# Performance work log

Hardware: AMD Instinct MI355X
Metric: run time of the kernel (lower is better)

## Reference

```python
import jax, jax.numpy as jnp
import numpy as np

N = 50000      # nodes
E = 800000     # edges (before self-loops)
DIN = 2        # dim_input
DEMB = 128     # dim_embedding
H = 8          # n_heads
DV = 16        # dim_values (H*DV == DEMB)
DH = 512       # dim_hidden
L = 2          # n_att_layers
K = 10         # APPNP steps
ALPHA = 0.1
EPS = 1e-5     # BatchNorm eps
NEG_SLOPE = 0.2  # GAT leaky_relu slope


def setup_inputs() -> dict:
    key = jax.random.key(0)
    ks = jax.random.split(key, 16)
    s = 0.05
    inp = {}
    inp["x"] = jax.random.normal(ks[0], (N, DIN), jnp.float32)
    inp["J"] = jax.random.uniform(ks[1], (N, 1), jnp.float32)
    inp["edge_index"] = jax.random.randint(ks[2], (2, E), 0, N, jnp.int32)
    # Lin1: Linear(dim_input+1, dim_embedding)
    inp["lin0_w"] = jax.random.normal(ks[3], (DIN + 1, DEMB), jnp.float32) * s
    inp["lin0_b"] = jnp.zeros((DEMB,), jnp.float32)
    # Per attention layer (stacked over L):
    inp["gat_w"]   = jax.random.normal(ks[4], (L, DEMB, H * DV), jnp.float32) * s
    inp["att_src"] = jax.random.normal(ks[5], (L, H, DV), jnp.float32) * s
    inp["att_dst"] = jax.random.normal(ks[6], (L, H, DV), jnp.float32) * s
    inp["lin1_w"]  = jax.random.normal(ks[7], (L, DV, DEMB), jnp.float32) * s
    inp["bn1_g"]   = jnp.ones((L, DEMB), jnp.float32)
    inp["bn1_b"]   = jnp.zeros((L, DEMB), jnp.float32)
    inp["lin2_w"]  = jax.random.normal(ks[8], (L, DEMB, DH), jnp.float32) * s
    inp["lin2_b"]  = jnp.zeros((L, DH), jnp.float32)
    inp["lin3_w"]  = jax.random.normal(ks[9], (L, DH, DEMB), jnp.float32) * s
    inp["lin3_b"]  = jnp.zeros((L, DEMB), jnp.float32)
    inp["bn2_g"]   = jnp.ones((L, DEMB), jnp.float32)
    inp["bn2_b"]   = jnp.zeros((L, DEMB), jnp.float32)
    return inp


def _bn(z, g, b):
    # BatchNorm1d over nodes, training-mode batch statistics (biased var)
    mu = z.mean(0)
    var = jnp.mean((z - mu) ** 2, axis=0)
    return g * (z - mu) * jax.lax.rsqrt(var + EPS) + b


def reference(x, J, edge_index, lin0_w, lin0_b, gat_w, att_src, att_dst,
              lin1_w, bn1_g, bn1_b, lin2_w, lin2_b, lin3_w, lin3_b,
              bn2_g, bn2_b):
    # add self-loops (PyG GATConv and APPNP defaults)
    loop = jnp.arange(N, dtype=edge_index.dtype)
    src = jnp.concatenate([edge_index[0], loop])  # message source j
    dst = jnp.concatenate([edge_index[1], loop])  # message target i

    h = jnp.concatenate([x, J], axis=1) @ lin0_w + lin0_b  # [N, DEMB]

    for l in range(L):
        # ---- GATConv ----
        xl = (h @ gat_w[l]).reshape(N, H, DV)                # [N,H,DV]
        a_s = (xl * att_src[l]).sum(-1)                      # [N,H]
        a_d = (xl * att_dst[l]).sum(-1)                      # [N,H]
        e = jax.nn.leaky_relu(a_s[src] + a_d[dst], NEG_SLOPE)  # [E',H]
        e = e - jax.ops.segment_max(e, dst, num_segments=N)[dst]
        ee = jnp.exp(e)
        alpha = ee / jax.ops.segment_sum(ee, dst, num_segments=N)[dst]
        msg = xl[src] * alpha[:, :, None]                    # [E',H,DV]
        gat_out = jax.ops.segment_sum(msg, dst, num_segments=N)  # [N,H,DV]
        # lin1 per head then sum over heads
        hsum = jnp.einsum('nhc,cd->nd', gat_out, lin1_w[l])  # [N,DEMB]
        h1 = _bn(h + hsum, bn1_g[l], bn1_b[l])
        h2 = jax.nn.relu(h1 @ lin2_w[l] + lin2_b[l]) @ lin3_w[l] + lin3_b[l]
        h = _bn(h2 + h1, bn2_g[l], bn2_b[l])

    # ---- APPNP: K steps of (1-a)*Ahat h + a*h0, Ahat = D^-1/2 (A+I) D^-1/2 ----
    deg = jax.ops.segment_sum(jnp.ones_like(dst, jnp.float32), dst, num_segments=N)
    dinv = jax.lax.rsqrt(jnp.maximum(deg, 1.0))  # self-loops guarantee deg>=1
    norm = (dinv[src] * dinv[dst])[:, None]      # [E',1]
    h0 = h

    def step(hk, _):
        agg = jax.ops.segment_sum(norm * hk[src], dst, num_segments=N)
        return (1.0 - ALPHA) * agg + ALPHA * h0, None

    h, _ = jax.lax.scan(step, h, None, length=K)
    return jnp.concatenate([h, J], axis=1)  # [N, DEMB+1]
```

## Files before the change

### kernel.cpp

```cpp
#include <hip/hip_runtime.h>

#define NN 50000
#define NP 50048
#define NMT64 782
#define NE 800000
#define EP (NE + NN)
#define DEMB 128
#define DHID 512
#define NB_SCAN 196

typedef unsigned short ushort_t;
typedef __attribute__((ext_vector_type(8))) short short8_t;
typedef __attribute__((ext_vector_type(4))) float float4_t;

__device__ __forceinline__ float bf2f(ushort_t u) {
    return __uint_as_float(((unsigned int)u) << 16);
}
__device__ __forceinline__ ushort_t f2bf(float f) {
    unsigned int x = __float_as_uint(f);
    x += 0x7fffu + ((x >> 16) & 1u);
    return (ushort_t)(x >> 16);
}
__device__ __forceinline__ float lo16(unsigned int w) { return __uint_as_float(w << 16); }
__device__ __forceinline__ float hi16(unsigned int w) { return __uint_as_float(w & 0xffff0000u); }
__device__ __forceinline__ unsigned int pack2(float a, float b) {
    return (unsigned int)f2bf(a) | ((unsigned int)f2bf(b) << 16);
}
__device__ __forceinline__ void gl_lds16(const ushort_t* g, ushort_t* l) {
    __builtin_amdgcn_global_load_lds(
        (const __attribute__((address_space(1))) void*)g,
        (__attribute__((address_space(3))) void*)l, 16, 0, 0);
}
static inline int cdiv(int a, int b) { return (a + b - 1) / b; }

__global__ void k_detect(const unsigned int* __restrict__ Jw, int* __restrict__ flag) {
    if (threadIdx.x != 0 || blockIdx.x != 0) return;
    int votes = 0;
    for (int i = 0; i < 8; ++i) {
        unsigned int w = Jw[i];
        unsigned int ex = (w >> 23) & 0xFFu;
        if ((w >> 31) == 0u && ex >= 100u && ex <= 126u) votes++;
    }
    *flag = (votes >= 6) ? 1 : 0;
}

struct CvtArgs {
    const void* src[16];
    float* dst[16];
    int n[16];
};
__global__ void k_cvt_all(CvtArgs a, const int* __restrict__ flag) {
    int which = blockIdx.y;
    int i = blockIdx.x * 256 + threadIdx.x;
    if (i >= a.n[which]) return;
    float v;
    if (*flag) v = ((const float*)a.src[which])[i];
    else       v = bf2f(((const ushort_t*)a.src[which])[i]);
    a.dst[which][i] = v;
}

struct TrArgs {
    const float* src[6];
    ushort_t* dst[6];
    int K[6];
    int Nc[6];
    int perm[6];
};
__global__ void k_tr_all(TrArgs a) {
    int which = blockIdx.y;
    int idx = blockIdx.x * 256 + threadIdx.x;
    int K = a.K[which], Nc = a.Nc[which];
    if (idx >= K * Nc) return;
    int k = idx / Nc, n = idx - k * Nc;
    int kd = k;
    if (a.perm[which]) {
        int kk = k & 63;
        kd = (k & ~63) | ((kk & 32) + 2 * (kk & 15) + ((kk >> 4) & 1));
    }
    a.dst[which][n * K + kd] = f2bf(a.src[which][idx]);
}

__global__ void k_deg(const int* __restrict__ ei, int* __restrict__ deg) {
    int e = blockIdx.x * 256 + threadIdx.x;
    if (e >= EP) return;
    int d = (e < NE) ? ei[NE + e] : (e - NE);
    atomicAdd(&deg[d], 1);
}

__global__ void k_part(const int* __restrict__ deg, int* __restrict__ part) {
    __shared__ int sm[256];
    int i = blockIdx.x * 256 + threadIdx.x;
    int v = (i < NN) ? deg[i] : 0;
    sm[threadIdx.x] = v;
    __syncthreads();
    for (int off = 128; off > 0; off >>= 1) {
        if (threadIdx.x < off) sm[threadIdx.x] += sm[threadIdx.x + off];
        __syncthreads();
    }
    if (threadIdx.x == 0) part[blockIdx.x] = sm[0];
}

__global__ void k_scan2(const int* __restrict__ part, int* __restrict__ poff,
                        int* __restrict__ rowp) {
    __shared__ int sm[256];
    int t = threadIdx.x;
    int v = (t < NB_SCAN) ? part[t] : 0;
    sm[t] = v;
    __syncthreads();
    int incl = v;
    for (int off = 1; off < 256; off <<= 1) {
        int u = (t >= off) ? sm[t - off] : 0;
        __syncthreads();
        incl += u;
        sm[t] = incl;
        __syncthreads();
    }
    if (t < NB_SCAN) poff[t] = incl - v;
    if (t == 255) rowp[NN] = sm[255];
}

__global__ void k_rowp(const int* __restrict__ deg, const int* __restrict__ poff,
                       int* __restrict__ rowp, float* __restrict__ dinv,
                       int* __restrict__ fill) {
    __shared__ int sm[256];
    int i = blockIdx.x * 256 + threadIdx.x;
    int t = threadIdx.x;
    int v = (i < NN) ? deg[i] : 0;
    sm[t] = v;
    __syncthreads();
    int incl = v;
    for (int off = 1; off < 256; off <<= 1) {
        int u = (t >= off) ? sm[t - off] : 0;
        __syncthreads();
        incl += u;
        sm[t] = incl;
        __syncthreads();
    }
    if (i < NN) {
        int rp = poff[blockIdx.x] + incl - v;
        rowp[i] = rp;
        fill[i] = rp;
        dinv[i] = rsqrtf(fmaxf((float)v, 1.0f));
    }
}

__global__ void k_fill(const int* __restrict__ ei, int* __restrict__ fillpos,
                       ushort_t* __restrict__ col) {
    int e = blockIdx.x * 256 + threadIdx.x;
    if (e >= EP) return;
    int s, d;
    if (e < NE) { s = ei[e]; d = ei[NE + e]; } else { s = d = e - NE; }
    int pos = atomicAdd(&fillpos[d], 1);
    col[pos] = (ushort_t)s;
}

__global__ void k_lin0(const float* __restrict__ x, const float* __restrict__ J,
                       const float* __restrict__ w, const float* __restrict__ b,
                       ushort_t* __restrict__ hB) {
    int idx = blockIdx.x * 256 + threadIdx.x;
    if (idx >= NN * DEMB) return;
    int n = idx >> 7, d = idx & 127;
    float v = x[n * 2] * w[d] + x[n * 2 + 1] * w[DEMB + d] + J[n] * w[2 * DEMB + d] + b[d];
    hB[idx] = f2bf(v);
}

__global__ void k_att(const unsigned int* __restrict__ xlB, const float* __restrict__ asrc,
                      const float* __restrict__ adst, float* __restrict__ a_s,
                      float* __restrict__ a_d) {
    int idx = blockIdx.x * 256 + threadIdx.x;
    if (idx >= NN * 8) return;
    int n = idx >> 3, hh = idx & 7;
    const unsigned int* row = xlB + (size_t)n * 64 + hh * 8;
    float s = 0.f, d = 0.f;
#pragma unroll
    for (int c = 0; c < 8; ++c) {
        unsigned int w = row[c];
        float v0 = lo16(w), v1 = hi16(w);
        s += v0 * asrc[hh * 16 + 2 * c] + v1 * asrc[hh * 16 + 2 * c + 1];
        d += v0 * adst[hh * 16 + 2 * c] + v1 * adst[hh * 16 + 2 * c + 1];
    }
    a_s[idx] = s;
    a_d[idx] = d;
}

__global__ __launch_bounds__(256) void k_z1s(const ushort_t* __restrict__ hB,
                                             const float* __restrict__ g,
                                             const float* __restrict__ w1,
                                             float* __restrict__ stats) {
    int d = threadIdx.x & 127;
    int rstart = blockIdx.x * 2 + (threadIdx.x >> 7);
    int stride = gridDim.x * 2;
    float s1 = 0.f, s2 = 0.f;
    for (int r = rstart; r < NN; r += stride) {
        const float* gr = g + r * 16;
        float s = bf2f(hB[(size_t)r * DEMB + d]);
#pragma unroll
        for (int c = 0; c < 16; ++c) s += gr[c] * w1[c * DEMB + d];
        s1 += s;
        s2 += s * s;
    }
    __shared__ float b1[256], b2[256];
    b1[threadIdx.x] = s1;
    b2[threadIdx.x] = s2;
    __syncthreads();
    if (threadIdx.x < 128) {
        atomicAdd(&stats[threadIdx.x], b1[threadIdx.x] + b1[threadIdx.x + 128]);
        atomicAdd(&stats[128 + threadIdx.x], b2[threadIdx.x] + b2[threadIdx.x + 128]);
    }
}

__global__ void k_bnapply1(const ushort_t* __restrict__ hB, const float* __restrict__ g,
                           const float* __restrict__ w1, const float* __restrict__ stats,
                           const float* __restrict__ gam, const float* __restrict__ bet,
                           ushort_t* __restrict__ outB) {
    int idx = blockIdx.x * 256 + threadIdx.x;
    if (idx >= NN * DEMB) return;
    int n = idx >> 7, d = idx & 127;
    float s = bf2f(hB[idx]);
    const float* gr = g + n * 16;
#pragma unroll
    for (int c = 0; c < 16; ++c) s += gr[c] * w1[c * DEMB + d];
    const float invN = 1.0f / (float)NN;
    float mu = stats[d] * invN;
    float var = stats[128 + d] * invN - mu * mu;
    float rs = rsqrtf(fmaxf(var, 0.f) + 1e-5f);
    float v = gam[d] * (s - mu) * rs + bet[d];
    outB[idx] = f2bf(v);
}

__global__ void k_bnapply(const ushort_t* __restrict__ zB, const float* __restrict__ stats,
                          const float* __restrict__ gam, const float* __restrict__ bet,
                          ushort_t* __restrict__ outB) {
    int idx = blockIdx.x * 256 + threadIdx.x;
    if (idx >= NN * DEMB) return;
    int d = idx & 127;
    const float invN = 1.0f / (float)NN;
    float mu = stats[d] * invN;
    float var = stats[128 + d] * invN - mu * mu;
    float rs = rsqrtf(fmaxf(var, 0.f) + 1e-5f);
    float v = gam[d] * (bf2f(zB[idx]) - mu) * rs + bet[d];
    outB[idx] = f2bf(v);
}

__global__ void k_bnapply_fin(const unsigned int* __restrict__ zB, const float* __restrict__ stats,
                              const float* __restrict__ gam, const float* __restrict__ bet,
                              const float* __restrict__ dinv,
                              unsigned int* __restrict__ hs, unsigned int* __restrict__ h0p) {
    int idx = blockIdx.x * 256 + threadIdx.x;
    if (idx >= NN * 64) return;
    int n = idx >> 6, j = idx & 63;
    int d0 = j * 2;
    const float invN = 1.0f / (float)NN;
    unsigned int zw = zB[idx];
    float z0 = lo16(zw), z1 = hi16(zw);
    float mu0 = stats[d0] * invN, mu1 = stats[d0 + 1] * invN;
    float v0 = stats[128 + d0] * invN - mu0 * mu0;
    float v1 = stats[128 + d0 + 1] * invN - mu1 * mu1;
    float rs0 = rsqrtf(fmaxf(v0, 0.f) + 1e-5f);
    float rs1 = rsqrtf(fmaxf(v1, 0.f) + 1e-5f);
    float a = gam[d0] * (z0 - mu0) * rs0 + bet[d0];
    float b = gam[d0 + 1] * (z1 - mu1) * rs1 + bet[d0 + 1];
    float di = dinv[n];
    int q = j >> 4, dd = j & 15;
    size_t o = (size_t)q * NN * 16 + (size_t)n * 16 + dd;
    hs[o] = pack2(di * a, di * b);
    h0p[o] = pack2(a, b);
}

__global__ __launch_bounds__(256) void k_gat(const int* __restrict__ rowp,
                                             const ushort_t* __restrict__ col,
                                             const float* __restrict__ a_s, const float* __restrict__ a_d,
                                             const unsigned int* __restrict__ xlB, float* __restrict__ g) {
    int wid = (blockIdx.x * 256 + threadIdx.x) >> 6;
    int lane = threadIdx.x & 63;
    if (wid >= NN) return;
    int p0 = rowp[wid], p1 = rowp[wid + 1];
    int hh = lane >> 3;
    float ad2 = a_d[wid * 8 + hh];
    float acc0 = 0.f, acc1 = 0.f, s = 0.f;
    int p = p0;
    while (p < p1) {
        int cnt = p1 - p;
        if (cnt > 64) cnt = 64;
        int pl = p + lane;
        int jv = (int)col[pl < p1 ? pl : (p1 - 1)];
        int i = 0;
        for (; i + 8 <= cnt; i += 8) {
            int j0 = __shfl(jv, i),     j1 = __shfl(jv, i + 1);
            int j2 = __shfl(jv, i + 2), j3 = __shfl(jv, i + 3);
            int j4 = __shfl(jv, i + 4), j5 = __shfl(jv, i + 5);
            int j6 = __shfl(jv, i + 6), j7 = __shfl(jv, i + 7);
            float e0 = a_s[j0 * 8 + hh] + ad2, e1 = a_s[j1 * 8 + hh] + ad2;
            float e2 = a_s[j2 * 8 + hh] + ad2, e3 = a_s[j3 * 8 + hh] + ad2;
            float e4 = a_s[j4 * 8 + hh] + ad2, e5 = a_s[j5 * 8 + hh] + ad2;
            float e6 = a_s[j6 * 8 + hh] + ad2, e7 = a_s[j7 * 8 + hh] + ad2;
            unsigned int w0 = xlB[j0 * 64 + lane], w1 = xlB[j1 * 64 + lane];
            unsigned int w2 = xlB[j2 * 64 + lane], w3 = xlB[j3 * 64 + lane];
            unsigned int w4 = xlB[j4 * 64 + lane], w5 = xlB[j5 * 64 + lane];
            unsigned int w6 = xlB[j6 * 64 + lane], w7 = xlB[j7 * 64 + lane];
            e0 = e0 > 0.f ? e0 : 0.2f * e0;  e1 = e1 > 0.f ? e1 : 0.2f * e1;
            e2 = e2 > 0.f ? e2 : 0.2f * e2;  e3 = e3 > 0.f ? e3 : 0.2f * e3;
            e4 = e4 > 0.f ? e4 : 0.2f * e4;  e5 = e5 > 0.f ? e5 : 0.2f * e5;
            e6 = e6 > 0.f ? e6 : 0.2f * e6;  e7 = e7 > 0.f ? e7 : 0.2f * e7;
            float al0 = __expf(e0), al1 = __expf(e1), al2 = __expf(e2), al3 = __expf(e3);
            float al4 = __expf(e4), al5 = __expf(e5), al6 = __expf(e6), al7 = __expf(e7);
            s += al0 + al1 + al2 + al3 + al4 + al5 + al6 + al7;
            acc0 += al0 * lo16(w0) + al1 * lo16(w1) + al2 * lo16(w2) + al3 * lo16(w3) +
                    al4 * lo16(w4) + al5 * lo16(w5) + al6 * lo16(w6) + al7 * lo16(w7);
            acc1 += al0 * hi16(w0) + al1 * hi16(w1) + al2 * hi16(w2) + al3 * hi16(w3) +
                    al4 * hi16(w4) + al5 * hi16(w5) + al6 * hi16(w6) + al7 * hi16(w7);
        }
        for (; i < cnt; ++i) {
            int j = __shfl(jv, i);
            float e = a_s[j * 8 + hh] + ad2;
            e = e > 0.f ? e : 0.2f * e;
            float al = __expf(e);
            unsigned int w = xlB[j * 64 + lane];
            s += al;
            acc0 += al * lo16(w);
            acc1 += al * hi16(w);
        }
        p += cnt;
    }
    float inv = 1.f / s;
    acc0 *= inv;
    acc1 *= inv;
    acc0 += __shfl_xor(acc0, 8);  acc1 += __shfl_xor(acc1, 8);
    acc0 += __shfl_xor(acc0, 16); acc1 += __shfl_xor(acc1, 16);
    acc0 += __shfl_xor(acc0, 32); acc1 += __shfl_xor(acc1, 32);
    if (lane < 8) ((float2*)g)[wid * 8 + lane] = make_float2(acc0, acc1);
}

__global__ __launch_bounds__(256) void k_appnp(const int* __restrict__ rowp,
                                               const ushort_t* __restrict__ col,
                                               const float* __restrict__ dinv,
                                               const unsigned int* __restrict__ hs,
                                               const unsigned int* __restrict__ h0p,
                                               unsigned int* __restrict__ hs_out,
                                               const float* __restrict__ Jf,
                                               const int* __restrict__ flag,
                                               void* __restrict__ out, int writeOut) {
    int b = blockIdx.x;
    int w = threadIdx.x >> 6, lane = threadIdx.x & 63;
    int s = (b & 7) >> 1;
    int g = ((b >> 3) << 1) + (b & 1);
    int ns = lane >> 4, d = lane & 15;
    int n = g * 16 + w * 4 + ns;
    int valid = (n < NN);
    int nc = valid ? n : (NN - 1);
    int p0 = rowp[nc], p1 = rowp[nc + 1];
    const unsigned int* hsq = hs + (size_t)s * NN * 16;
    unsigned int hw = h0p[(size_t)s * NN * 16 + (size_t)nc * 16 + d];
    float di = dinv[nc];
    int base = ns << 4;
    float a0 = 0.f, a1 = 0.f;
    int p = p0;
    while (p < p1) {
        int cnt = p1 - p;
        if (cnt > 16) cnt = 16;
        int pl = p + d;
        int jv = (int)col[pl < p1 ? pl : (p1 - 1)];
        int lim = cnt - 1;
        for (int k = 0; k < cnt; k += 8) {
            int q0 = k,     q1 = k + 1, q2 = k + 2, q3 = k + 3;
            int q4 = k + 4, q5 = k + 5, q6 = k + 6, q7 = k + 7;
            int j0 = __shfl(jv, base + (q0 < lim ? q0 : lim));
            int j1 = __shfl(jv, base + (q1 < lim ? q1 : lim));
            int j2 = __shfl(jv, base + (q2 < lim ? q2 : lim));
            int j3 = __shfl(jv, base + (q3 < lim ? q3 : lim));
            int j4 = __shfl(jv, base + (q4 < lim ? q4 : lim));
            int j5 = __shfl(jv, base + (q5 < lim ? q5 : lim));
            int j6 = __shfl(jv, base + (q6 < lim ? q6 : lim));
            int j7 = __shfl(jv, base + (q7 < lim ? q7 : lim));
            unsigned int w0 = hsq[j0 * 16 + d], w1 = hsq[j1 * 16 + d];
            unsigned int w2 = hsq[j2 * 16 + d], w3 = hsq[j3 * 16 + d];
            unsigned int w4 = hsq[j4 * 16 + d], w5 = hsq[j5 * 16 + d];
            unsigned int w6 = hsq[j6 * 16 + d], w7 = hsq[j7 * 16 + d];
            a0 += ((q0 <= lim) ? lo16(w0) : 0.f) + ((q1 <= lim) ? lo16(w1) : 0.f) +
                  ((q2 <= lim) ? lo16(w2) : 0.f) + ((q3 <= lim) ? lo16(w3) : 0.f) +
                  ((q4 <= lim) ? lo16(w4) : 0.f) + ((q5 <= lim) ? lo16(w5) : 0.f) +
                  ((q6 <= lim) ? lo16(w6) : 0.f) + ((q7 <= lim) ? lo16(w7) : 0.f);
            a1 += ((q0 <= lim) ? hi16(w0) : 0.f) + ((q1 <= lim) ? hi16(w1) : 0.f) +
                  ((q2 <= lim) ? hi16(w2) : 0.f) + ((q3 <= lim) ? hi16(w3) : 0.f) +
                  ((q4 <= lim) ? hi16(w4) : 0.f) + ((q5 <= lim) ? hi16(w5) : 0.f) +
                  ((q6 <= lim) ? hi16(w6) : 0.f) + ((q7 <= lim) ? hi16(w7) : 0.f);
        }
        p += cnt;
    }
    float n0 = 0.9f * di * a0 + 0.1f * lo16(hw);
    float n1 = 0.9f * di * a1 + 0.1f * hi16(hw);
    if (valid) {
        if (!writeOut) {
            hs_out[(size_t)s * NN * 16 + (size_t)n * 16 + d] = pack2(di * n0, di * n1);
        } else {
            size_t obase = (size_t)n * 129 + s * 32 + 2 * d;
            if (*flag) {
                float* o = (float*)out;
                o[obase] = n0;
                o[obase + 1] = n1;
                if (s == 0 && d == 0) o[(size_t)n * 129 + 128] = Jf[n];
            } else {
                ushort_t* o = (ushort_t*)out;
                o[obase] = f2bf(n0);
                o[obase + 1] = f2bf(n1);
                if (s == 0 && d == 0) o[(size_t)n * 129 + 128] = f2bf(Jf[n]);
            }
        }
    }
}

template <int MODE>
__global__ __launch_bounds__(256) void k_gemm64(const ushort_t* __restrict__ A,
                                                const ushort_t* __restrict__ Bt,
                                                int M, int K, int Nc,
                                                const float* __restrict__ bias,
                                                const ushort_t* __restrict__ res,
                                                ushort_t* __restrict__ outB,
                                                float* __restrict__ stats) {
    __shared__ __align__(16) ushort_t lsA[2][64 * 32];
    __shared__ __align__(16) ushort_t lsB[2][128 * 32];
    int t = threadIdx.x;
    int m0 = blockIdx.x * 64;
    int n0 = blockIdx.y * 128;
    int w = t >> 6, lane = t & 63;
    int row16 = lane & 15, quad = lane >> 4;
    int nbase = w * 32;
    float4_t acc[8];
#pragma unroll
    for (int i = 0; i < 8; ++i) acc[i] = (float4_t){0.f, 0.f, 0.f, 0.f};
    int lrow = lane >> 2;
    int lcol = (lane & 3) * 8;
    const ushort_t* gA  = A  + (size_t)(m0 + w * 16 + lrow) * K + lcol;
    const ushort_t* gB0 = Bt + (size_t)(n0 + w * 32 + lrow) * K + lcol;
    const ushort_t* gB1 = Bt + (size_t)(n0 + w * 32 + 16 + lrow) * K + lcol;
    ushort_t* dA  = &lsA[0][0] + (w * 16) * 32;
    ushort_t* dB0 = &lsB[0][0] + (w * 32) * 32;
    ushort_t* dB1 = &lsB[0][0] + (w * 32 + 16) * 32;
    const int bufStrideA = 64 * 32, bufStrideB = 128 * 32;
    const int nK = K >> 5;
    gl_lds16(gA, dA);
    gl_lds16(gB0, dB0);
    gl_lds16(gB1, dB1);
    for (int kb = 0; kb < nK; ++kb) {
        __syncthreads();
        int nb = kb + 1;
        if (nb < nK) {
            int b = nb & 1;
            int k0 = nb << 5;
            gl_lds16(gA + k0, dA + b * bufStrideA);
            gl_lds16(gB0 + k0, dB0 + b * bufStrideB);
            gl_lds16(gB1 + k0, dB1 + b * bufStrideB);
        }
        const ushort_t* la = &lsA[kb & 1][0];
        const ushort_t* lb = &lsB[kb & 1][0];
        short8_t afr[4], bfr[2];
#pragma unroll
        for (int i = 0; i < 4; ++i)
            afr[i] = *(const short8_t*)(la + (i * 16 + row16) * 32 + quad * 8);
#pragma unroll
        for (int i = 0; i < 2; ++i)
            bfr[i] = *(const short8_t*)(lb + (nbase + i * 16 + row16) * 32 + quad * 8);
#pragma unroll
        for (int mt = 0; mt < 4; ++mt)
#pragma unroll
            for (int nt = 0; nt < 2; ++nt)
                acc[mt * 2 + nt] = __builtin_amdgcn_mfma_f32_16x16x32_bf16(
                    afr[mt], bfr[nt], acc[mt * 2 + nt], 0, 0, 0);
    }
#pragma unroll
    for (int mt = 0; mt < 4; ++mt) {
#pragma unroll
        for (int nt = 0; nt < 2; ++nt) {
            int cc = n0 + nbase + nt * 16 + row16;
#pragma unroll
            for (int r = 0; r < 4; ++r) {
                int rr = m0 + mt * 16 + quad * 4 + r;
                if (rr < M) {
                    outB[(size_t)rr * Nc + cc] = f2bf(acc[mt * 2 + nt][r]);
                }
            }
        }
    }
}

__global__ __launch_bounds__(256, 3) void k_ffn(const ushort_t* __restrict__ A,
                                                const ushort_t* __restrict__ W2t,
                                                const ushort_t* __restrict__ W3t,
                                                const float* __restrict__ b2,
                                                const float* __restrict__ b3,
                                                const ushort_t* __restrict__ res,
                                                ushort_t* __restrict__ outB,
                                                float* __restrict__ stats) {
    __shared__ __align__(16) ushort_t sW2[4 * 64 * 32];
    __shared__ __align__(16) ushort_t sW3[2 * 128 * 32];
    __shared__ __align__(16) ushort_t sAH[4 * 2048];
    int t = threadIdx.x;
    int w = t >> 6, lane = t & 63;
    int wm = w >> 1, wn = w & 1;
    int m0 = blockIdx.x * 64;
    int row16 = lane & 15, quad = lane >> 4;
    int sw = (row16 >> 2) & 3;
    int srow = lane >> 2;
    int klin = lane & 3;

#pragma unroll
    for (int i = 0; i < 4; ++i) {
        int row = i * 16 + srow;
        int kc = klin ^ ((row >> 2) & 3);
        gl_lds16(A + (size_t)(m0 + row) * 128 + w * 32 + kc * 8,
                 sAH + w * 2048 + i * 512);
        gl_lds16(W2t + (size_t)row * 128 + w * 32 + kc * 8,
                 sW2 + w * 2048 + i * 512);
        int f = w * 4 + i;
        int ks = f >> 3;
        int n3 = (f & 7) * 16 + srow;
        int kc3 = klin ^ ((n3 >> 2) & 3);
        gl_lds16(W3t + (size_t)n3 * 512 + ks * 32 + kc3 * 8,
                 sW3 + f * 512);
    }
    __syncthreads();

    short8_t afrA[2][4];
#pragma unroll
    for (int mt = 0; mt < 2; ++mt)
#pragma unroll
        for (int kb = 0; kb < 4; ++kb)
            afrA[mt][kb] = *(const short8_t*)(sAH + kb * 2048 +
                                              (wm * 32 + mt * 16 + row16) * 32 + (quad ^ sw) * 8);
    __syncthreads();

    char* Hb = (char*)sAH;
    float* s1 = (float*)(Hb + 8192);
    float* s2 = s1 + 128;
    if (t < 128) { s1[t] = 0.f; s2[t] = 0.f; }

    float4_t accz[2][4];
#pragma unroll
    for (int mt = 0; mt < 2; ++mt)
#pragma unroll
        for (int nt = 0; nt < 4; ++nt) accz[mt][nt] = (float4_t){0.f, 0.f, 0.f, 0.f};

    for (int c = 0; c < 8; ++c) {
        float b20 = b2[c * 64 + wn * 32 + row16];
        float b21 = b2[c * 64 + wn * 32 + 16 + row16];
        float4_t acch[2][2];
#pragma unroll
        for (int mt = 0; mt < 2; ++mt)
#pragma unroll
            for (int nt = 0; nt < 2; ++nt) acch[mt][nt] = (float4_t){0.f, 0.f, 0.f, 0.f};
#pragma unroll
        for (int kb = 0; kb < 4; ++kb) {
            short8_t b0 = *(const short8_t*)(sW2 + kb * 2048 +
                                             (wn * 32 + row16) * 32 + (quad ^ sw) * 8);
            short8_t b1 = *(const short8_t*)(sW2 + kb * 2048 +
                                             (wn * 32 + 16 + row16) * 32 + (quad ^ sw) * 8);
            acch[0][0] = __builtin_amdgcn_mfma_f32_16x16x32_bf16(afrA[0][kb], b0, acch[0][0], 0, 0, 0);
            acch[0][1] = __builtin_amdgcn_mfma_f32_16x16x32_bf16(afrA[0][kb], b1, acch[0][1], 0, 0, 0);
            acch[1][0] = __builtin_amdgcn_mfma_f32_16x16x32_bf16(afrA[1][kb], b0, acch[1][0], 0, 0, 0);
            acch[1][1] = __builtin_amdgcn_mfma_f32_16x16x32_bf16(afrA[1][kb], b1, acch[1][1], 0, 0, 0);
        }
#pragma unroll
        for (int mt = 0; mt < 2; ++mt) {
#pragma unroll
            for (int r = 0; r < 4; ++r) {
                int row = wm * 32 + mt * 16 + quad * 4 + r;
                int d = wn * 16 + row16;
                int byteOff = row * 128 + ((((d >> 2) ^ (row & 7))) << 4) + (d & 3) * 4;
                float v0 = acch[mt][0][r] + b20; v0 = v0 > 0.f ? v0 : 0.f;
                float v1 = acch[mt][1][r] + b21; v1 = v1 > 0.f ? v1 : 0.f;
                *(unsigned int*)(Hb + byteOff) = pack2(v0, v1);
            }
        }
        __syncthreads();
        if (c < 7) {
#pragma unroll
            for (int i = 0; i < 4; ++i) {
                int n = i * 16 + srow;
                int kc = klin ^ ((n >> 2) & 3);
                gl_lds16(W2t + (size_t)((c + 1) * 64 + n) * 128 + w * 32 + kc * 8,
                         sW2 + w * 2048 + i * 512);
            }
        }
#pragma unroll
        for (int ks = 0; ks < 2; ++ks) {
            short8_t afrH[2];
#pragma unroll
            for (int mt = 0; mt < 2; ++mt)
                afrH[mt] = *(const short8_t*)(Hb + (wm * 32 + mt * 16 + row16) * 128 +
                                              (((ks * 4 + quad) ^ (row16 & 7)) << 4));
#pragma unroll
            for (int nt = 0; nt < 4; ++nt) {
                short8_t bfr = *(const short8_t*)(sW3 + ks * 4096 +
                                                  (wn * 64 + nt * 16 + row16) * 32 + (quad ^ sw) * 8);
                accz[0][nt] = __builtin_amdgcn_mfma_f32_16x16x32_bf16(afrH[0], bfr, accz[0][nt], 0, 0, 0);
                accz[1][nt] = __builtin_amdgcn_mfma_f32_16x16x32_bf16(afrH[1], bfr, accz[1][nt], 0, 0, 0);
            }
        }
        __syncthreads();
        if (c < 7) {
#pragma unroll
            for (int i = 0; i < 4; ++i) {
                int f = w * 4 + i;
                int ks = f >> 3;
                int n = (f & 7) * 16 + srow;
                int kc = klin ^ ((n >> 2) & 3);
                gl_lds16(W3t + (size_t)n * 512 + (c + 1) * 64 + ks * 32 + kc * 8,
                         sW3 + f * 512);
            }
        }
    }

#pragma unroll
    for (int mt = 0; mt < 2; ++mt) {
#pragma unroll
        for (int nt = 0; nt < 4; ++nt) {
            int cc = wn * 64 + nt * 16 + row16;
            float bv = b3[cc];
            float ls = 0.f, lq = 0.f;
#pragma unroll
            for (int r = 0; r < 4; ++r) {
                int rr = m0 + wm * 32 + mt * 16 + quad * 4 + r;
                if (rr < NN) {
                    float v = accz[mt][nt][r] + bv + bf2f(res[(size_t)rr * 128 + cc]);
                    outB[(size_t)rr * 128 + cc] = f2bf(v);
                    ls += v;
                    lq += v * v;
                }
            }
            atomicAdd(&s1[cc], ls);
            atomicAdd(&s2[cc], lq);
        }
    }
    __syncthreads();
    if (t < 128) {
        atomicAdd(&stats[t], s1[t]);
        atomicAdd(&stats[128 + t], s2[t]);
    }
}

extern "C" void kernel_launch(void* const* d_in, const int* in_sizes, int n_in,
                              void* d_out, int out_size, void* d_ws, size_t ws_size,
                              hipStream_t stream) {
    const int* ei = (const int*)d_in[2];

    char* p = (char*)d_ws;
    auto alloc = [&](size_t bytes) {
        void* r = (void*)p;
        p += (bytes + 255) & ~(size_t)255;
        return r;
    };
    ushort_t* hB    = (ushort_t*)alloc((size_t)NP * DEMB * 2);
    ushort_t* h1B   = (ushort_t*)alloc((size_t)NP * DEMB * 2);
    ushort_t* xlB   = (ushort_t*)alloc((size_t)NN * DEMB * 2);
    unsigned int* hsA  = (unsigned int*)alloc((size_t)NN * 64 * 4);
    unsigned int* hsB_ = (unsigned int*)alloc((size_t)NN * 64 * 4);
    unsigned int* h0p  = (unsigned int*)alloc((size_t)NN * 64 * 4);
    float*    asv   = (float*)alloc((size_t)NN * 8 * 4);
    float*    adv   = (float*)alloc((size_t)NN * 8 * 4);
    float*    gv    = (float*)alloc((size_t)NN * 16 * 4);
    float*    dinvv = (float*)alloc((size_t)NN * 4);
    float*    stats = (float*)alloc(4 * 256 * 4);
    int*      deg   = (int*)alloc((size_t)NN * 4);
    int*      rowp  = (int*)alloc((size_t)(NN + 1) * 4);
    int*      fill  = (int*)alloc((size_t)NN * 4);
    ushort_t* colv  = (ushort_t*)alloc((size_t)EP * 2);
    int*      part  = (int*)alloc(NB_SCAN * 4);
    int*      poff  = (int*)alloc(NB_SCAN * 4);
    int*      flag  = (int*)alloc(256);
    ushort_t* wtg   = (ushort_t*)alloc((size_t)2 * 128 * 128 * 2);
    ushort_t* wt2   = (ushort_t*)alloc((size_t)2 * 512 * 128 * 2);
    ushort_t* wt3   = (ushort_t*)alloc((size_t)2 * 128 * 512 * 2);
    float* xf   = (float*)alloc((size_t)NN * 2 * 4);
    float* Jf   = (float*)alloc((size_t)NN * 4);
    float* l0wF = (float*)alloc(384 * 4);
    float* l0bF = (float*)alloc(128 * 4);
    float* gwF  = (float*)alloc(32768 * 4);
    float* asF  = (float*)alloc(256 * 4);
    float* adF  = (float*)alloc(256 * 4);
    float* w1F  = (float*)alloc(4096 * 4);
    float* b1gF = (float*)alloc(256 * 4);
    float* b1bF = (float*)alloc(256 * 4);
    float* w2F  = (float*)alloc(131072 * 4);
    float* b2F  = (float*)alloc(1024 * 4);
    float* w3F  = (float*)alloc(131072 * 4);
    float* b3F  = (float*)alloc(256 * 4);
    float* b2gF = (float*)alloc(256 * 4);
    float* b2bF = (float*)alloc(256 * 4);

    k_detect<<<1, 64, 0, stream>>>((const unsigned int*)d_in[1], flag);
    CvtArgs ca;
    {
        const int srcIdx[16] = {0, 1, 3, 4, 5, 6, 7, 8, 9, 10, 11, 12, 13, 14, 15, 16};
        float* dsts[16] = {xf, Jf, l0wF, l0bF, gwF, asF, adF, w1F, b1gF, b1bF,
                           w2F, b2F, w3F, b3F, b2gF, b2bF};
        const int ns[16] = {NN * 2, NN, 384, 128, 32768, 256, 256, 4096, 256, 256,
                            131072, 1024, 131072, 256, 256, 256};
        for (int i = 0; i < 16; ++i) { ca.src[i] = d_in[srcIdx[i]]; ca.dst[i] = dsts[i]; ca.n[i] = ns[i]; }
    }
    k_cvt_all<<<dim3(cdiv(131072, 256), 16), 256, 0, stream>>>(ca, flag);

    hipMemsetAsync(deg, 0, (size_t)NN * 4, stream);
    hipMemsetAsync(stats, 0, 4 * 256 * 4, stream);
    k_deg<<<cdiv(EP, 256), 256, 0, stream>>>(ei, deg);
    k_part<<<NB_SCAN, 256, 0, stream>>>(deg, part);
    k_scan2<<<1, 256, 0, stream>>>(part, poff, rowp);
    k_rowp<<<NB_SCAN, 256, 0, stream>>>(deg, poff, rowp, dinvv, fill);
    k_fill<<<cdiv(EP, 256), 256, 0, stream>>>(ei, fill, colv);

    TrArgs ta;
    {
        const float* srcs[6] = {gwF, gwF + 16384, w2F, w2F + 65536, w3F, w3F + 65536};
        ushort_t* dsts[6] = {wtg, wtg + 16384, wt2, wt2 + 65536, wt3, wt3 + 65536};
        const int Ks[6] = {128, 128, 128, 128, 512, 512};
        const int Ncs[6] = {128, 128, 512, 512, 128, 128};
        const int perms[6] = {0, 0, 0, 0, 1, 1};
        for (int i = 0; i < 6; ++i) {
            ta.src[i] = srcs[i]; ta.dst[i] = dsts[i]; ta.K[i] = Ks[i]; ta.Nc[i] = Ncs[i];
            ta.perm[i] = perms[i];
        }
    }
    k_tr_all<<<dim3(cdiv(65536, 256), 6), 256, 0, stream>>>(ta);

    k_lin0<<<cdiv(NN * DEMB, 256), 256, 0, stream>>>(xf, Jf, l0wF, l0bF, hB);

    for (int l = 0; l < 2; ++l) {
        float* st1 = stats + (l * 2 + 0) * 256;
        float* st2 = stats + (l * 2 + 1) * 256;
        ushort_t* zB = xlB;
        k_gemm64<3><<<dim3(NMT64, 1), 256, 0, stream>>>(hB, wtg + l * 16384, NN, 128, 128,
                                                        nullptr, nullptr, xlB, nullptr);
        k_att<<<cdiv(NN * 8, 256), 256, 0, stream>>>((const unsigned int*)xlB, asF + l * 128,
                                                     adF + l * 128, asv, adv);
        k_gat<<<cdiv(NN * 64, 256), 256, 0, stream>>>(rowp, colv, asv, adv,
                                                      (const unsigned int*)xlB, gv);
        k_z1s<<<512, 256, 0, stream>>>(hB, gv, w1F + l * 2048, st1);
        k_bnapply1<<<cdiv(NN * DEMB, 256), 256, 0, stream>>>(hB, gv, w1F + l * 2048, st1,
                                                             b1gF + l * 128, b1bF + l * 128,
                                                             h1B);
        k_ffn<<<NMT64, 256, 0, stream>>>(h1B, wt2 + l * 65536, wt3 + l * 65536,
                                         b2F + l * 512, b3F + l * 128, h1B, zB, st2);
        if (l == 0) {
            k_bnapply<<<cdiv(NN * DEMB, 256), 256, 0, stream>>>(zB, st2, b2gF, b2bF, hB);
        } else {
            k_bnapply_fin<<<cdiv(NN * 64, 256), 256, 0, stream>>>((const unsigned int*)zB, st2,
                                                                  b2gF + 128, b2bF + 128,
                                                                  dinvv, hsA, h0p);
        }
    }

    unsigned int* pin = hsA;
    unsigned int* pout = hsB_;
    for (int k = 0; k < 10; ++k) {
        int last = (k == 9) ? 1 : 0;
        k_appnp<<<12504, 256, 0, stream>>>(rowp, colv, dinvv, pin, h0p, pout,
                                           Jf, flag, d_out, last);
        unsigned int* tmp = pout;
        pout = pin;
        pin = tmp;
    }
}
```

Before: 893.8 us.

## Pad CSR rows to multiples of eight with zero sentinel node for APPNP

Rounds every CSR row length up to a multiple of 8 and fills the padding with a sentinel column index pointing at an added zeroed row in the APPNP feature buffers. The APPNP gather loop can then drop per-element bounds clamping and masking, and it processes fixed groups of 8 neighbours. GAT keeps the true degree so its softmax is unchanged. The cost is extra gathers of the sentinel row, a larger col array, and two small setup kernels.

```diff
diff --git a/kernel.cpp b/kernel.cpp
--- a/kernel.cpp
+++ b/kernel.cpp
@@ -1,10 +1,12 @@
 #include <hip/hip_runtime.h>
 
 #define NN 50000
+#define NN1 50001
 #define NP 50048
 #define NMT64 782
 #define NE 800000
 #define EP (NE + NN)
+#define EPP_MAX (EP + 7 * NN + 64)
 #define DEMB 128
 #define DHID 512
 #define NB_SCAN 196
@@ -91,6 +93,7 @@
     __shared__ int sm[256];
     int i = blockIdx.x * 256 + threadIdx.x;
     int v = (i < NN) ? deg[i] : 0;
+    v = (v + 7) & ~7;
     sm[threadIdx.x] = v;
     __syncthreads();
     for (int off = 128; off > 0; off >>= 1) {
@@ -125,7 +128,8 @@
     __shared__ int sm[256];
     int i = blockIdx.x * 256 + threadIdx.x;
     int t = threadIdx.x;
-    int v = (i < NN) ? deg[i] : 0;
+    int rv = (i < NN) ? deg[i] : 0;
+    int v = (rv + 7) & ~7;
     sm[t] = v;
     __syncthreads();
     int incl = v;
@@ -140,7 +144,7 @@
         int rp = poff[blockIdx.x] + incl - v;
         rowp[i] = rp;
         fill[i] = rp;
-        dinv[i] = rsqrtf(fmaxf((float)v, 1.0f));
+        dinv[i] = rsqrtf(fmaxf((float)rv, 1.0f));
     }
 }
 
@@ -152,6 +156,23 @@
     if (e < NE) { s = ei[e]; d = ei[NE + e]; } else { s = d = e - NE; }
     int pos = atomicAdd(&fillpos[d], 1);
     col[pos] = (ushort_t)s;
+}
+
+__global__ void k_pad(const int* __restrict__ fillpos, const int* __restrict__ rowp,
+                      ushort_t* __restrict__ col) {
+    int n = blockIdx.x * 256 + threadIdx.x;
+    if (n >= NN) return;
+    int p = fillpos[n], p1 = rowp[n + 1];
+    for (; p < p1; ++p) col[p] = (ushort_t)NN;
+}
+
+__global__ void k_zsent(unsigned int* __restrict__ a, unsigned int* __restrict__ b) {
+    int t = threadIdx.x;
+    if (t >= 64) return;
+    int s = t >> 4, d = t & 15;
+    size_t o = (size_t)s * NN1 * 16 + (size_t)NN * 16 + d;
+    a[o] = 0;
+    b[o] = 0;
 }
 
 __global__ void k_lin0(const float* __restrict__ x, const float* __restrict__ J,
@@ -262,19 +283,20 @@
     float b = gam[d0 + 1] * (z1 - mu1) * rs1 + bet[d0 + 1];
     float di = dinv[n];
     int q = j >> 4, dd = j & 15;
-    size_t o = (size_t)q * NN * 16 + (size_t)n * 16 + dd;
+    size_t o = (size_t)q * NN1 * 16 + (size_t)n * 16 + dd;
     hs[o] = pack2(di * a, di * b);
     h0p[o] = pack2(a, b);
 }
 
 __global__ __launch_bounds__(256) void k_gat(const int* __restrict__ rowp,
+                                             const int* __restrict__ deg,
                                              const ushort_t* __restrict__ col,
                                              const float* __restrict__ a_s, const float* __restrict__ a_d,
                                              const unsigned int* __restrict__ xlB, float* __restrict__ g) {
     int wid = (blockIdx.x * 256 + threadIdx.x) >> 6;
     int lane = threadIdx.x & 63;
     if (wid >= NN) return;
-    int p0 = rowp[wid], p1 = rowp[wid + 1];
+    int p0 = rowp[wid], p1 = p0 + deg[wid];
     int hh = lane >> 3;
     float ad2 = a_d[wid * 8 + hh];
     float acc0 = 0.f, acc1 = 0.f, s = 0.f;
@@ -349,49 +371,50 @@
     int valid = (n < NN);
     int nc = valid ? n : (NN - 1);
     int p0 = rowp[nc], p1 = rowp[nc + 1];
-    const unsigned int* hsq = hs + (size_t)s * NN * 16;
-    unsigned int hw = h0p[(size_t)s * NN * 16 + (size_t)nc * 16 + d];
+    const unsigned int* hsq = hs + (size_t)s * NN1 * 16;
+    unsigned int hw = h0p[(size_t)s * NN1 * 16 + (size_t)nc * 16 + d];
     float di = dinv[nc];
     int base = ns << 4;
     float a0 = 0.f, a1 = 0.f;
     int p = p0;
     while (p < p1) {
-        int cnt = p1 - p;
-        if (cnt > 16) cnt = 16;
-        int pl = p + d;
-        int jv = (int)col[pl < p1 ? pl : (p1 - 1)];
-        int lim = cnt - 1;
-        for (int k = 0; k < cnt; k += 8) {
-            int q0 = k,     q1 = k + 1, q2 = k + 2, q3 = k + 3;
-            int q4 = k + 4, q5 = k + 5, q6 = k + 6, q7 = k + 7;
-            int j0 = __shfl(jv, base + (q0 < lim ? q0 : lim));
-            int j1 = __shfl(jv, base + (q1 < lim ? q1 : lim));
-            int j2 = __shfl(jv, base + (q2 < lim ? q2 : lim));
-            int j3 = __shfl(jv, base + (q3 < lim ? q3 : lim));
-            int j4 = __shfl(jv, base + (q4 < lim ? q4 : lim));
-            int j5 = __shfl(jv, base + (q5 < lim ? q5 : lim));
-            int j6 = __shfl(jv, base + (q6 < lim ? q6 : lim));
-            int j7 = __shfl(jv, base + (q7 < lim ? q7 : lim));
+        int rem = p1 - p;
+        int jv = (int)col[p + d];
+        {
+            int j0 = __shfl(jv, base + 0), j1 = __shfl(jv, base + 1);
+            int j2 = __shfl(jv, base + 2), j3 = __shfl(jv, base + 3);
+            int j4 = __shfl(jv, base + 4), j5 = __shfl(jv, base + 5);
+            int j6 = __shfl(jv, base + 6), j7 = __shfl(jv, base + 7);
             unsigned int w0 = hsq[j0 * 16 + d], w1 = hsq[j1 * 16 + d];
             unsigned int w2 = hsq[j2 * 16 + d], w3 = hsq[j3 * 16 + d];
             unsigned int w4 = hsq[j4 * 16 + d], w5 = hsq[j5 * 16 + d];
             unsigned int w6 = hsq[j6 * 16 + d], w7 = hsq[j7 * 16 + d];
-            a0 += ((q0 <= lim) ? lo16(w0) : 0.f) + ((q1 <= lim) ? lo16(w1) : 0.f) +
-                  ((q2 <= lim) ? lo16(w2) : 0.f) + ((q3 <= lim) ? lo16(w3) : 0.f) +
-                  ((q4 <= lim) ? lo16(w4) : 0.f) + ((q5 <= lim) ? lo16(w5) : 0.f) +
-                  ((q6 <= lim) ? lo16(w6) : 0.f) + ((q7 <= lim) ? lo16(w7) : 0.f);
-            a1 += ((q0 <= lim) ? hi16(w0) : 0.f) + ((q1 <= lim) ? hi16(w1) : 0.f) +
-                  ((q2 <= lim) ? hi16(w2) : 0.f) + ((q3 <= lim) ? hi16(w3) : 0.f) +
-                  ((q4 <= lim) ? hi16(w4) : 0.f) + ((q5 <= lim) ? hi16(w5) : 0.f) +
-                  ((q6 <= lim) ? hi16(w6) : 0.f) + ((q7 <= lim) ? hi16(w7) : 0.f);
-        }
-        p += cnt;
+            a0 += lo16(w0) + lo16(w1) + lo16(w2) + lo16(w3) +
+                  lo16(w4) + lo16(w5) + lo16(w6) + lo16(w7);
+            a1 += hi16(w0) + hi16(w1) + hi16(w2) + hi16(w3) +
+                  hi16(w4) + hi16(w5) + hi16(w6) + hi16(w7);
+        }
+        if (rem > 8) {
+            int j0 = __shfl(jv, base + 8),  j1 = __shfl(jv, base + 9);
+            int j2 = __shfl(jv, base + 10), j3 = __shfl(jv, base + 11);
+            int j4 = __shfl(jv, base + 12), j5 = __shfl(jv, base + 13);
+            int j6 = __shfl(jv, base + 14), j7 = __shfl(jv, base + 15);
+            unsigned int w0 = hsq[j0 * 16 + d], w1 = hsq[j1 * 16 + d];
+            unsigned int w2 = hsq[j2 * 16 + d], w3 = hsq[j3 * 16 + d];
+            unsigned int w4 = hsq[j4 * 16 + d], w5 = hsq[j5 * 16 + d];
+            unsigned int w6 = hsq[j6 * 16 + d], w7 = hsq[j7 * 16 + d];
+            a0 += lo16(w0) + lo16(w1) + lo16(w2) + lo16(w3) +
+                  lo16(w4) + lo16(w5) + lo16(w6) + lo16(w7);
+            a1 += hi16(w0) + hi16(w1) + hi16(w2) + hi16(w3) +
+                  hi16(w4) + hi16(w5) + hi16(w6) + hi16(w7);
+        }
+        p += 16;
     }
     float n0 = 0.9f * di * a0 + 0.1f * lo16(hw);
     float n1 = 0.9f * di * a1 + 0.1f * hi16(hw);
     if (valid) {
         if (!writeOut) {
-            hs_out[(size_t)s * NN * 16 + (size_t)n * 16 + d] = pack2(di * n0, di * n1);
+            hs_out[(size_t)s * NN1 * 16 + (size_t)n * 16 + d] = pack2(di * n0, di * n1);
         } else {
             size_t obase = (size_t)n * 129 + s * 32 + 2 * d;
             if (*flag) {
@@ -652,9 +675,9 @@
     ushort_t* hB    = (ushort_t*)alloc((size_t)NP * DEMB * 2);
     ushort_t* h1B   = (ushort_t*)alloc((size_t)NP * DEMB * 2);
     ushort_t* xlB   = (ushort_t*)alloc((size_t)NN * DEMB * 2);
-    unsigned int* hsA  = (unsigned int*)alloc((size_t)NN * 64 * 4);
-    unsigned int* hsB_ = (unsigned int*)alloc((size_t)NN * 64 * 4);
-    unsigned int* h0p  = (unsigned int*)alloc((size_t)NN * 64 * 4);
+    unsigned int* hsA  = (unsigned int*)alloc((size_t)4 * NN1 * 16 * 4);
+    unsigned int* hsB_ = (unsigned int*)alloc((size_t)4 * NN1 * 16 * 4);
+    unsigned int* h0p  = (unsigned int*)alloc((size_t)4 * NN1 * 16 * 4);
     float*    asv   = (float*)alloc((size_t)NN * 8 * 4);
     float*    adv   = (float*)alloc((size_t)NN * 8 * 4);
     float*    gv    = (float*)alloc((size_t)NN * 16 * 4);
@@ -663,7 +686,7 @@
     int*      deg   = (int*)alloc((size_t)NN * 4);
     int*      rowp  = (int*)alloc((size_t)(NN + 1) * 4);
     int*      fill  = (int*)alloc((size_t)NN * 4);
-    ushort_t* colv  = (ushort_t*)alloc((size_t)EP * 2);
+    ushort_t* colv  = (ushort_t*)alloc((size_t)EPP_MAX * 2);
     int*      part  = (int*)alloc(NB_SCAN * 4);
     int*      poff  = (int*)alloc(NB_SCAN * 4);
     int*      flag  = (int*)alloc(256);
@@ -706,6 +729,8 @@
     k_scan2<<<1, 256, 0, stream>>>(part, poff, rowp);
     k_rowp<<<NB_SCAN, 256, 0, stream>>>(deg, poff, rowp, dinvv, fill);
     k_fill<<<cdiv(EP, 256), 256, 0, stream>>>(ei, fill, colv);
+    k_pad<<<cdiv(NN, 256), 256, 0, stream>>>(fill, rowp, colv);
+    k_zsent<<<1, 64, 0, stream>>>(hsA, hsB_);
 
     TrArgs ta;
     {
@@ -731,7 +756,7 @@
                                                         nullptr, nullptr, xlB, nullptr);
         k_att<<<cdiv(NN * 8, 256), 256, 0, stream>>>((const unsigned int*)xlB, asF + l * 128,
                                                      adF + l * 128, asv, adv);
-        k_gat<<<cdiv(NN * 64, 256), 256, 0, stream>>>(rowp, colv, asv, adv,
+        k_gat<<<cdiv(NN * 64, 256), 256, 0, stream>>>(rowp, deg, colv, asv, adv,
                                                       (const unsigned int*)xlB, gv);
         k_z1s<<<512, 256, 0, stream>>>(hB, gv, w1F + l * 2048, st1);
         k_bnapply1<<<cdiv(NN * DEMB, 256), 256, 0, stream>>>(hB, gv, w1F + l * 2048, st1,
```

New measurement: 823.4 us. -7.9%, faster.
